# Kernel optimization log

Hardware: AMD Instinct MI355X
Metric: run time of the kernel (lower is better)

The kernel has to match this reference:

```python
import jax, jax.numpy as jnp
import numpy as np

B, R, VIS, MM, E, ATT, D, V, MAXLEN = 128, 36, 2048, 1024, 512, 512, 1024, 10000, 20


def setup_inputs() -> dict:
    key = jax.random.key(0)
    ks = jax.random.split(key, 16)
    s = 0.02
    visual = jax.random.normal(ks[0], (B, R, VIS), jnp.float32)
    joint = jax.random.normal(ks[1], (B, MM), jnp.float32)
    captions = jax.random.randint(ks[2], (B, MAXLEN), 0, V)
    # torch code requires lengths sorted descending (prefix slicing)
    lengths = jnp.sort(jax.random.randint(ks[3], (B,), 1, MAXLEN + 1))[::-1].astype(jnp.int32)
    embed_W = (jax.random.normal(ks[4], (V, E), jnp.float32) * s).at[0].set(0.0)  # padding_idx=0
    Wih = jax.random.normal(ks[5], (4 * D, E + VIS), jnp.float32) * s
    bih = jnp.zeros((4 * D,), jnp.float32)
    Whh = jax.random.normal(ks[6], (4 * D, D), jnp.float32) * s
    bhh = jnp.zeros((4 * D,), jnp.float32)
    W_init_h = jax.random.normal(ks[7], (D, MM), jnp.float32) * s
    b_init_h = jnp.zeros((D,), jnp.float32)
    W_init_c = jax.random.normal(ks[8], (D, MM), jnp.float32) * s
    b_init_c = jnp.zeros((D,), jnp.float32)
    Wv = jax.random.normal(ks[9], (ATT, VIS), jnp.float32) * s
    Wh = jax.random.normal(ks[10], (ATT, D), jnp.float32) * s
    att_bias = jnp.zeros((R,), jnp.float32)
    Ww = jax.random.normal(ks[11], (1, ATT), jnp.float32) * s
    Wout = jax.random.normal(ks[12], (V, D), jnp.float32) * s
    bout = jnp.zeros((V,), jnp.float32)
    return dict(visual=visual, joint=joint, captions=captions, lengths=lengths, max_len=MAXLEN,
                embed_W=embed_W, Wih=Wih, bih=bih, Whh=Whh, bhh=bhh,
                W_init_h=W_init_h, b_init_h=b_init_h, W_init_c=W_init_c, b_init_c=b_init_c,
                Wv=Wv, Wh=Wh, att_bias=att_bias, Ww=Ww, Wout=Wout, bout=bout)


def reference(visual, joint, captions, lengths, max_len, embed_W, Wih, bih, Whh, bhh,
              W_init_h, b_init_h, W_init_c, b_init_c, Wv, Wh, att_bias, Ww, Wout, bout):
    T = max_len - 1  # python int -> static scan length
    # dropout treated as identity (eval mode)
    words_seq = embed_W[captions[:, :T]]            # [B, T, E]
    h0 = joint @ W_init_h.T + b_init_h              # [B, D]
    c0 = joint @ W_init_c.T + b_init_c
    feas0 = visual.mean(axis=1)                     # [B, VIS]  (step 0 context)
    att_fea = jnp.einsum('brv,av->bra', visual, Wv)  # precompute visual projection
    lens = lengths.astype(jnp.int32)

    def step(carry, xs):
        h, c = carry
        t, words = xs
        # attention over 36 regions (used only when t != 0)
        ah = h @ Wh.T                                                   # [B, A]
        full = jax.nn.relu(att_fea + ah[:, None, :] + att_bias[None, :, None])
        alpha = jax.nn.softmax(jnp.einsum('bra,a->br', full, Ww[0]), axis=-1)
        ctx = jnp.einsum('br,brv->bv', alpha, visual)
        feas = jnp.where(t == 0, feas0, ctx)
        x = jnp.concatenate([feas, words], axis=-1)                     # [B, VIS+E]
        gates = x @ Wih.T + bih + h @ Whh.T + bhh                       # [B, 4D]
        i_, f_, g_, o_ = jnp.split(gates, 4, axis=-1)
        c_new = jax.nn.sigmoid(f_) * c + jax.nn.sigmoid(i_) * jnp.tanh(g_)
        h_new = jax.nn.sigmoid(o_) * jnp.tanh(c_new)
        mask = (t < lens)[:, None]                                      # ragged mask == torch prefix slice
        out = h_new @ Wout.T + bout                                     # [B, V]
        return (jnp.where(mask, h_new, h), jnp.where(mask, c_new, c)), jnp.where(mask, out, 0.0)

    _, preds = jax.lax.scan(step, (h0, c0), (jnp.arange(T), jnp.swapaxes(words_seq, 0, 1)))
    return jnp.transpose(preds, (1, 0, 2))  # [B, T, V]
```

## Files before the change

kernel.cpp:

```cpp
#include <hip/hip_runtime.h>
#include <math.h>

#define B 128
#define R 36
#define VIS 2048
#define MM 1024
#define E 512
#define ATT 512
#define D 1024
#define V 10000
#define MAXLEN 20
#define T 19
#define G4 4096

typedef unsigned short bf16_t;
typedef __attribute__((ext_vector_type(8))) short short8;
typedef __attribute__((ext_vector_type(4))) float f32x4;
typedef __attribute__((ext_vector_type(4))) unsigned short ushort4v;

__device__ __forceinline__ bf16_t f2bf(float f) {
    unsigned u = __float_as_uint(f);
    u += 0x7fff + ((u >> 16) & 1);
    return (bf16_t)(u >> 16);
}
__device__ __forceinline__ float bf2f(bf16_t b) {
    return __uint_as_float(((unsigned)b) << 16);
}
__device__ __forceinline__ float sigmoidf_(float x) { return 1.0f / (1.0f + expf(-x)); }

__device__ __forceinline__ void stage16(const bf16_t* g, bf16_t* lds_wave_base, int lane) {
#if defined(__has_builtin) && __has_builtin(__builtin_amdgcn_global_load_lds)
    __builtin_amdgcn_global_load_lds(
        (const __attribute__((address_space(1))) void*)g,
        (__attribute__((address_space(3))) void*)lds_wave_base, 16, 0, 0);
#else
    *(short8*)(lds_wave_base + lane * 8) = *(const short8*)g;
#endif
}

template<int MODE>
__global__ __launch_bounds__(256) void mfma_gemm_lds(
    const bf16_t* __restrict__ A, const bf16_t* __restrict__ W,
    const float* __restrict__ bias, const int* __restrict__ lengths,
    float* __restrict__ C, int M, int N, int K, int ldc,
    const float* __restrict__ bias2, float* __restrict__ C2,
    bf16_t* __restrict__ C3)
{
    __shared__ __align__(16) bf16_t As[128 * 32];
    __shared__ __align__(16) bf16_t Ws[128 * 32];
    const int tid = threadIdx.x;
    const int wave = tid >> 6, lane = tid & 63;
    const int wm = wave >> 1, wn = wave & 1;
    const int quad = lane >> 4, l16 = lane & 15;
    const int m0 = blockIdx.y * 128;
    const int n0 = blockIdx.x * 128;
    if (MODE == 2 && n0 >= N) return;

    int cnt = 128;
    if constexpr (MODE == 2) {
        const int tt = blockIdx.y;
        cnt = __syncthreads_count(tid < B && lengths[tid] > tt);
    }

    f32x4 acc[4][4];
    #pragma unroll
    for (int i = 0; i < 4; ++i)
        #pragma unroll
        for (int j = 0; j < 4; ++j)
            acc[i][j] = (f32x4){0.f, 0.f, 0.f, 0.f};

    for (int kk = 0; kk < K; kk += 32) {
        #pragma unroll
        for (int i = 0; i < 2; ++i) {
            int c = tid + i * 256;
            int row = c >> 2, seg = c & 3;
            if (MODE != 2 || (i * 64 + wave * 16) < cnt) {
                int m = m0 + row; if (m >= M) m = M - 1;
                stage16(A + (size_t)m * K + kk + seg * 8, &As[(i * 256 + wave * 64) * 8], lane);
            }
            int n = n0 + row; if (n >= N) n = N - 1;
            stage16(W + (size_t)n * K + kk + seg * 8, &Ws[(i * 256 + wave * 64) * 8], lane);
        }
        __syncthreads();
        short8 af[4], bfr[4];
        #pragma unroll
        for (int fm = 0; fm < 4; ++fm) {
            const int rt = (MODE == 2) ? fm * 2 + wm : wm * 4 + fm;
            if (MODE != 2 || rt * 16 < cnt)
                af[fm] = *(const short8*)&As[(rt * 16 + l16) * 32 + quad * 8];
        }
        #pragma unroll
        for (int fn = 0; fn < 4; ++fn)
            bfr[fn] = *(const short8*)&Ws[(wn * 64 + fn * 16 + l16) * 32 + quad * 8];
        #pragma unroll
        for (int fm = 0; fm < 4; ++fm) {
            const int rt = (MODE == 2) ? fm * 2 + wm : wm * 4 + fm;
            if (MODE == 2 && rt * 16 >= cnt) continue;
            #pragma unroll
            for (int fn = 0; fn < 4; ++fn)
                acc[fm][fn] = __builtin_amdgcn_mfma_f32_16x16x32_bf16(
                    af[fm], bfr[fn], acc[fm][fn], 0, 0, 0);
        }
        __syncthreads();
    }

    #pragma unroll
    for (int fm = 0; fm < 4; ++fm) {
        const int rt = (MODE == 2) ? fm * 2 + wm : wm * 4 + fm;
        #pragma unroll
        for (int fn = 0; fn < 4; ++fn) {
            #pragma unroll
            for (int r = 0; r < 4; ++r) {
                int m = m0 + rt * 16 + quad * 4 + r;
                int n = n0 + wn * 64 + fn * 16 + l16;
                if (m >= M || n >= N) continue;
                float v = acc[fm][fn][r];
                if (MODE == 0) {
                    if (bias) v += bias[n];
                    C[(size_t)m * ldc + n] = v;
                } else if (MODE == 2) {
                    int t = m >> 7, b = m & 127;
                    v = (t < lengths[b]) ? (v + bias[n]) : 0.f;
                    C[((size_t)b * T + t) * V + n] = v;
                } else if (MODE == 4) {
                    if (n < D) {
                        float v2 = v + bias[n];
                        C[(size_t)m * D + n] = v2;
                        C3[(size_t)m * D + n] = f2bf(v2);
                    } else {
                        C2[(size_t)m * D + (n - D)] = v + bias2[n - D];
                    }
                } else {
                    ((bf16_t*)C)[(size_t)m * ldc + n] = f2bf(v);
                }
            }
        }
    }
}

__global__ __launch_bounds__(256) void mfma_ah(
    const bf16_t* __restrict__ h_in,
    const bf16_t* __restrict__ Wh_pk,
    float* __restrict__ ah)
{
    __shared__ __align__(16) bf16_t Ws[32 * 1024];
    const int tid = threadIdx.x;
    const int wave = tid >> 6, lane = tid & 63;
    const int quad = lane >> 4, l16 = lane & 15;
    const int a0 = blockIdx.x * 32;
    const int m0 = blockIdx.y * 64;

    const bf16_t* slab = Wh_pk + ((size_t)blockIdx.x << 15);
    #pragma unroll
    for (int i = 0; i < 16; ++i) {
        int c = i * 256 + tid;
        stage16(slab + (size_t)c * 8, &Ws[(i * 256 + wave * 64) * 8], lane);
    }
    const bf16_t* Ar = h_in + (size_t)(m0 + wave * 16 + l16) * D + quad * 8;
    f32x4 acc0 = (f32x4){0.f, 0.f, 0.f, 0.f};
    f32x4 acc1 = (f32x4){0.f, 0.f, 0.f, 0.f};
    __syncthreads();

    #pragma unroll 8
    for (int kt = 0; kt < 32; ++kt) {
        short8 af = *(const short8*)(Ar + kt * 32);
        const int cb = (kt * 4 + quad) * 32 * 8;
        short8 b0 = *(const short8*)&Ws[cb + l16 * 8];
        short8 b1 = *(const short8*)&Ws[cb + (16 + l16) * 8];
        acc0 = __builtin_amdgcn_mfma_f32_16x16x32_bf16(af, b0, acc0, 0, 0, 0);
        acc1 = __builtin_amdgcn_mfma_f32_16x16x32_bf16(af, b1, acc1, 0, 0, 0);
    }
    #pragma unroll
    for (int r = 0; r < 4; ++r) {
        int m = m0 + wave * 16 + quad * 4 + r;
        ah[(size_t)m * ATT + a0 + l16]      = acc0[r];
        ah[(size_t)m * ATT + a0 + 16 + l16] = acc1[r];
    }
}

__global__ __launch_bounds__(256) void att_sc_p(
    const float* __restrict__ ah, const float* __restrict__ att_fea,
    const float* __restrict__ att_bias, const float* __restrict__ Ww,
    const bf16_t* __restrict__ P_bf, const float* __restrict__ wordsW,
    float* __restrict__ partial, int t)
{
    const int b = blockIdx.x, half = blockIdx.y, tid = threadIdx.x;
    __shared__ float ah_s[ATT];
    __shared__ float sc_s[64];
    __shared__ float alpha_s[R];
    const int wave = tid >> 6, lane = tid & 63;

    if (t > 0) {
        if (tid < 128) ((float4*)ah_s)[tid] = ((const float4*)(ah + (size_t)b * ATT))[tid];
        __syncthreads();
        for (int r = wave; r < R; r += 4) {
            float abv = att_bias[r];
            const float* af = att_fea + ((size_t)b * R + r) * ATT;
            float s = 0.f;
            for (int a = lane; a < ATT; a += 64) {
                float v = af[a] + ah_s[a] + abv;
                s = fmaf(fmaxf(v, 0.f), Ww[a], s);
            }
            #pragma unroll
            for (int off = 32; off; off >>= 1) s += __shfl_down(s, off);
            if (lane == 0) sc_s[r] = s;
        }
        __syncthreads();
        if (tid < 64) {
            float v = (tid < R) ? sc_s[tid] : -INFINITY;
            float m = v;
            #pragma unroll
            for (int off = 32; off; off >>= 1) m = fmaxf(m, __shfl_down(m, off));
            m = __shfl(m, 0);
            float e = (tid < R) ? expf(v - m) : 0.f;
            float ss = e;
            #pragma unroll
            for (int off = 32; off; off >>= 1) ss += __shfl_down(ss, off);
            ss = __shfl(ss, 0);
            if (tid < R) alpha_s[tid] = e / ss;
        }
        __syncthreads();
    }

    const int n0c = half * 2048 + tid * 8;
    float acc[8];
    #pragma unroll
    for (int j = 0; j < 8; ++j) acc[j] = 0.f;
    const bf16_t* Pb = P_bf + (size_t)b * R * G4 + n0c;
    #pragma unroll 4
    for (int r = 0; r < R; ++r) {
        float al = (t == 0) ? (1.0f / R) : alpha_s[r];
        short8 p = *(const short8*)(Pb + (size_t)r * G4);
        #pragma unroll
        for (int j = 0; j < 8; ++j)
            acc[j] = fmaf(al, bf2f((bf16_t)p[j]), acc[j]);
    }
    const float* wsl = wordsW + ((size_t)t * B + b) * G4 + n0c;
    float* po = partial + (size_t)b * G4 + n0c;
    float4 w0 = *(const float4*)(wsl);
    float4 w1 = *(const float4*)(wsl + 4);
    float4 o0 = { acc[0] + w0.x, acc[1] + w0.y, acc[2] + w0.z, acc[3] + w0.w };
    float4 o1 = { acc[4] + w1.x, acc[5] + w1.y, acc[6] + w1.z, acc[7] + w1.w };
    *(float4*)(po)     = o0;
    *(float4*)(po + 4) = o1;
}

__global__ __launch_bounds__(256) void whh_pack_k(
    const bf16_t* __restrict__ Whh, bf16_t* __restrict__ pk)
{
    int idx = blockIdx.x * 256 + threadIdx.x;
    int dt = idx >> 12, c = idx & 4095;
    int row = c & 31, qk = c >> 5;
    int rv = (row >> 3) * D + dt * 8 + (row & 7);
    *(short8*)(pk + ((size_t)dt << 15) + (size_t)c * 8) =
        *(const short8*)(Whh + (size_t)rv * D + qk * 8);
}

__global__ __launch_bounds__(256) void wh_pack_k(
    const bf16_t* __restrict__ Wh, bf16_t* __restrict__ pk)
{
    int idx = blockIdx.x * 256 + threadIdx.x;
    int at = idx >> 12, c = idx & 4095;
    int row = c & 31, qk = c >> 5;
    *(short8*)(pk + ((size_t)at << 15) + (size_t)c * 8) =
        *(const short8*)(Wh + (size_t)(at * 32 + row) * D + qk * 8);
}

__global__ __launch_bounds__(256) void gates_lstm(
    const bf16_t* __restrict__ h_in,
    const bf16_t* __restrict__ Whh_pk,
    const float* __restrict__ bih, const float* __restrict__ bhh,
    const float* __restrict__ partial,
    const int* __restrict__ lengths,
    float* __restrict__ c_st,
    float* __restrict__ h_f32,
    bf16_t* __restrict__ h_out,
    bf16_t* __restrict__ hseq,
    int t)
{
    __shared__ __align__(16) bf16_t Ws[32 * 1024];
    const int tid = threadIdx.x;
    const int wave = tid >> 6, lane = tid & 63;
    const int quad = lane >> 4, l16 = lane & 15;
    const int d0 = blockIdx.x * 8;
    const int m0 = blockIdx.y * 64;
    const int gsel_ = l16 >> 3, dr = l16 & 7;

    const bf16_t* slab = Whh_pk + ((size_t)blockIdx.x << 15);
    #pragma unroll
    for (int i = 0; i < 16; ++i) {
        int c = i * 256 + tid;
        stage16(slab + (size_t)c * 8, &Ws[(i * 256 + wave * 64) * 8], lane);
    }

    const bf16_t* Ar = h_in + (size_t)(m0 + wave * 16 + l16) * D + quad * 8;

    f32x4 acc0 = (f32x4){0.f, 0.f, 0.f, 0.f};
    f32x4 acc1 = (f32x4){0.f, 0.f, 0.f, 0.f};
    __syncthreads();

    #pragma unroll 8
    for (int kt = 0; kt < 32; ++kt) {
        short8 af = *(const short8*)(Ar + kt * 32);
        const int cb = (kt * 4 + quad) * 32 * 8;
        short8 b0 = *(const short8*)&Ws[cb + l16 * 8];
        short8 b1 = *(const short8*)&Ws[cb + (16 + l16) * 8];
        acc0 = __builtin_amdgcn_mfma_f32_16x16x32_bf16(af, b0, acc0, 0, 0, 0);
        acc1 = __builtin_amdgcn_mfma_f32_16x16x32_bf16(af, b1, acc1, 0, 0, 0);
    }

    const int d = d0 + dr;
    const int col0 = gsel_ * D + d;
    const int col1 = (2 + gsel_) * D + d;
    const float bia0 = bih[col0] + bhh[col0];
    const float bia1 = bih[col1] + bhh[col1];

    #pragma unroll
    for (int r = 0; r < 4; ++r) {
        int m = m0 + wave * 16 + quad * 4 + r;
        size_t pb = (size_t)m * G4;
        float v0 = acc0[r] + bia0 + partial[pb + col0];
        float v1 = acc1[r] + bia1 + partial[pb + col1];
        float w0 = __shfl_xor(v0, 8);
        float w1 = __shfl_xor(v1, 8);
        float iv, fv, gv, ov;
        if (gsel_ == 0) { iv = v0; gv = v1; fv = w0; ov = w1; }
        else            { fv = v0; ov = v1; iv = w0; gv = w1; }
        float ig = sigmoidf_(iv), fg = sigmoidf_(fv);
        float gg = tanhf(gv),     og = sigmoidf_(ov);
        size_t off = (size_t)m * D + d;
        if (gsel_ == 0) {
            float c_old = c_st[off];
            float h_old = h_f32[off];
            float cn = fmaf(fg, c_old, ig * gg);
            float hn = og * tanhf(cn);
            bool msk = t < lengths[m];
            float cv = msk ? cn : c_old;
            float hv = msk ? hn : h_old;
            c_st[off] = cv;
            h_f32[off] = hv;
            bf16_t hb = f2bf(hv);
            h_out[off] = hb;
            hseq[((size_t)t * B + m) * D + d] = hb;
        }
    }
}

struct CastSeg { const float* s; bf16_t* d; int cols; int ld; int total4; int blk0; };
struct Cast10 { CastSeg g[10]; };

__global__ __launch_bounds__(256) void fused_cast_k(Cast10 a)
{
    const int bx = blockIdx.x;
    CastSeg sg = a.g[0];
    #pragma unroll
    for (int j = 1; j < 10; ++j) if (bx >= a.g[j].blk0) sg = a.g[j];
    int idx = (bx - sg.blk0) * 256 + threadIdx.x;
    if (idx >= sg.total4) return;
    int cq = sg.cols >> 2;
    int r = idx / cq, c4 = (idx - r * cq) * 4;
    float4 v = *(const float4*)(sg.s + (size_t)r * sg.ld + c4);
    ushort4v o = { f2bf(v.x), f2bf(v.y), f2bf(v.z), f2bf(v.w) };
    *(ushort4v*)(sg.d + (size_t)r * sg.cols + c4) = o;
}

__global__ __launch_bounds__(128) void embed_k(
    const int* __restrict__ captions, const float* __restrict__ embed_W,
    bf16_t* __restrict__ words_bf)
{
    int bt = blockIdx.x;
    int b = bt / T, t = bt - b * T;
    int tok = captions[b * MAXLEN + t];
    int i = threadIdx.x * 4;
    float4 v = *(const float4*)(embed_W + (size_t)tok * E + i);
    ushort4v o = { f2bf(v.x), f2bf(v.y), f2bf(v.z), f2bf(v.w) };
    *(ushort4v*)(words_bf + ((size_t)t * B + b) * E + i) = o;
}

extern "C" void kernel_launch(void* const* d_in, const int* in_sizes, int n_in,
                              void* d_out, int out_size, void* d_ws, size_t ws_size,
                              hipStream_t stream) {
    const float* visual   = (const float*)d_in[0];
    const float* joint    = (const float*)d_in[1];
    const int*   captions = (const int*)d_in[2];
    const int*   lengths  = (const int*)d_in[3];
    const float* embed_W  = (const float*)d_in[5];
    const float* Wih      = (const float*)d_in[6];
    const float* bih      = (const float*)d_in[7];
    const float* Whh      = (const float*)d_in[8];
    const float* bhh      = (const float*)d_in[9];
    const float* W_init_h = (const float*)d_in[10];
    const float* b_init_h = (const float*)d_in[11];
    const float* W_init_c = (const float*)d_in[12];
    const float* b_init_c = (const float*)d_in[13];
    const float* Wv       = (const float*)d_in[14];
    const float* Wh       = (const float*)d_in[15];
    const float* att_bias = (const float*)d_in[16];
    const float* Ww       = (const float*)d_in[17];
    const float* Wout     = (const float*)d_in[18];
    const float* bout     = (const float*)d_in[19];
    float* out = (float*)d_out;

    char* cur = (char*)d_ws;
    auto alloc = [&](size_t bytes) { char* p = cur; cur += (bytes + 15) & ~size_t(15); return p; };
    float*  att_fea  = (float*)alloc((size_t)B * R * ATT * 4);
    float*  wordsW   = (float*)alloc((size_t)T * B * G4 * 4);
    float*  partial  = (float*)alloc((size_t)B * G4 * 4);
    float*  hf       = (float*)alloc((size_t)B * D * 4);
    float*  c_st     = (float*)alloc((size_t)B * D * 4);
    float*  ah       = (float*)alloc((size_t)B * ATT * 4);
    bf16_t* words_bf = (bf16_t*)alloc((size_t)T * B * E * 2);
    bf16_t* h_ping0  = (bf16_t*)alloc((size_t)B * D * 2);
    bf16_t* h_ping1  = (bf16_t*)alloc((size_t)B * D * 2);
    bf16_t* hseq_bf  = (bf16_t*)alloc((size_t)T * B * D * 2);
    bf16_t* P_bf     = (bf16_t*)alloc((size_t)B * R * G4 * 2);
    bf16_t* visual_bf= (bf16_t*)alloc((size_t)B * R * VIS * 2);
    bf16_t* Wv_bf    = (bf16_t*)alloc((size_t)ATT * VIS * 2);
    bf16_t* Wh_bf    = (bf16_t*)alloc((size_t)ATT * D * 2);
    bf16_t* Wh_pk    = (bf16_t*)alloc((size_t)ATT * D * 2);
    bf16_t* Whh_bf   = (bf16_t*)alloc((size_t)G4 * D * 2);
    bf16_t* Whh_pk   = (bf16_t*)alloc((size_t)G4 * D * 2);
    bf16_t* Wih_v_bf = (bf16_t*)alloc((size_t)G4 * VIS * 2);
    bf16_t* Wih_w_bf = (bf16_t*)alloc((size_t)G4 * E * 2);
    bf16_t* Wout_bf  = (bf16_t*)alloc((size_t)V * D * 2);
    bf16_t* joint_bf = (bf16_t*)alloc((size_t)B * MM * 2);
    bf16_t* Winit_bf = (bf16_t*)alloc((size_t)2 * D * MM * 2);

    Cast10 ca;
    int cum = 0;
    auto seg = [&](int i, const float* s, bf16_t* d, int rows, int cols, int ld) {
        int t4 = rows * (cols >> 2);
        ca.g[i] = { s, d, cols, ld, t4, cum };
        cum += (t4 + 255) / 256;
    };
    seg(0, visual, visual_bf, 1, B * R * VIS, B * R * VIS);
    seg(1, Wv,  Wv_bf,  ATT, VIS, VIS);
    seg(2, Wh,  Wh_bf,  ATT, D, D);
    seg(3, Whh, Whh_bf, G4, D, D);
    seg(4, Wih, Wih_v_bf, G4, VIS, VIS + E);
    seg(5, Wih + VIS, Wih_w_bf, G4, E, VIS + E);
    seg(6, Wout, Wout_bf, V, D, D);
    seg(7, joint, joint_bf, 1, B * MM, B * MM);
    seg(8, W_init_h, Winit_bf, 1, D * MM, D * MM);
    seg(9, W_init_c, Winit_bf + (size_t)D * MM, 1, D * MM, D * MM);
    fused_cast_k<<<cum, 256, 0, stream>>>(ca);

    whh_pack_k<<<(128 * 4096) / 256, 256, 0, stream>>>(Whh_bf, Whh_pk);
    wh_pack_k<<<(16 * 4096) / 256, 256, 0, stream>>>(Wh_bf, Wh_pk);
    embed_k<<<B * T, 128, 0, stream>>>(captions, embed_W, words_bf);

    mfma_gemm_lds<4><<<dim3(16, 1), 256, 0, stream>>>(
        joint_bf, Winit_bf, b_init_h, nullptr, hf, B, 2 * D, MM, D,
        b_init_c, c_st, h_ping0);

    mfma_gemm_lds<0><<<dim3(ATT / 128, (B * R) / 128), 256, 0, stream>>>(
        visual_bf, Wv_bf, nullptr, nullptr, att_fea, B * R, ATT, VIS, ATT,
        nullptr, nullptr, nullptr);

    mfma_gemm_lds<0><<<dim3(G4 / 128, (T * B) / 128), 256, 0, stream>>>(
        words_bf, Wih_w_bf, nullptr, nullptr, wordsW, T * B, G4, E, G4,
        nullptr, nullptr, nullptr);

    mfma_gemm_lds<3><<<dim3(G4 / 128, (B * R) / 128), 256, 0, stream>>>(
        visual_bf, Wih_v_bf, nullptr, nullptr, (float*)P_bf, B * R, G4, VIS, G4,
        nullptr, nullptr, nullptr);

    bf16_t* h_buf[2] = { h_ping0, h_ping1 };
    for (int t = 0; t < T; ++t) {
        if (t > 0)
            mfma_ah<<<dim3(ATT / 32, B / 64), 256, 0, stream>>>(
                h_buf[t & 1], Wh_pk, ah);
        att_sc_p<<<dim3(B, 2), 256, 0, stream>>>(
            ah, att_fea, att_bias, Ww, P_bf, wordsW, partial, t);
        gates_lstm<<<dim3(D / 8, B / 64), 256, 0, stream>>>(
            h_buf[t & 1], Whh_pk, bih, bhh, partial, lengths,
            c_st, hf, h_buf[(t + 1) & 1], hseq_bf, t);
    }

    mfma_gemm_lds<2><<<dim3(80, (T * B) / 128), 256, 0, stream>>>(
        hseq_bf, Wout_bf, bout, lengths, out, T * B, V, D, V,
        nullptr, nullptr, nullptr);
}
```

Measured before the change: 1.269 ms.

## Fuse attention scores into Wh GEMM and context into LSTM gates kernel

Each step's attention path is restructured. The scoring (relu, Ww dot) moves into the Wh MFMA kernel's epilogue, with per-tile partials combined by atomics into a per-step score buffer. The softmax, the alpha-weighted projected-context sum and the word term move into the gates kernel through a new d-tile-major packed layout of the visual×Wih product. This removes one kernel launch per step and the global round trips for ah and partial, at the cost of atomics, a memset and redundant softmax work per block. The MODE 2 staging skip for inactive rows is also dropped.

```diff
diff --git a/kernel.cpp b/kernel.cpp
--- a/kernel.cpp
+++ b/kernel.cpp
@@ -74,10 +74,8 @@
         for (int i = 0; i < 2; ++i) {
             int c = tid + i * 256;
             int row = c >> 2, seg = c & 3;
-            if (MODE != 2 || (i * 64 + wave * 16) < cnt) {
-                int m = m0 + row; if (m >= M) m = M - 1;
-                stage16(A + (size_t)m * K + kk + seg * 8, &As[(i * 256 + wave * 64) * 8], lane);
-            }
+            int m = m0 + row; if (m >= M) m = M - 1;
+            stage16(A + (size_t)m * K + kk + seg * 8, &As[(i * 256 + wave * 64) * 8], lane);
             int n = n0 + row; if (n >= N) n = N - 1;
             stage16(W + (size_t)n * K + kk + seg * 8, &Ws[(i * 256 + wave * 64) * 8], lane);
         }
@@ -130,6 +128,11 @@
                     } else {
                         C2[(size_t)m * D + (n - D)] = v + bias2[n - D];
                     }
+                } else if (MODE == 5) {
+                    int b = m / R, r2 = m - b * R;
+                    int dt = (n & 1023) >> 3;
+                    int c = ((n >> 10) << 3) | (n & 7);
+                    C3[((((size_t)dt * B + b) * R + r2) << 5) + c] = f2bf(v);
                 } else {
                     ((bf16_t*)C)[(size_t)m * ldc + n] = f2bf(v);
                 }
@@ -138,10 +141,10 @@
     }
 }
 
-__global__ __launch_bounds__(256) void mfma_ah(
-    const bf16_t* __restrict__ h_in,
-    const bf16_t* __restrict__ Wh_pk,
-    float* __restrict__ ah)
+__global__ __launch_bounds__(256) void ah_scores_k(
+    const bf16_t* __restrict__ h_in, const bf16_t* __restrict__ Wh_pk,
+    const float* __restrict__ att_fea, const float* __restrict__ att_bias,
+    const float* __restrict__ Ww, float* __restrict__ sc)
 {
     __shared__ __align__(16) bf16_t Ws[32 * 1024];
     const int tid = threadIdx.x;
@@ -170,131 +173,91 @@
         acc0 = __builtin_amdgcn_mfma_f32_16x16x32_bf16(af, b0, acc0, 0, 0, 0);
         acc1 = __builtin_amdgcn_mfma_f32_16x16x32_bf16(af, b1, acc1, 0, 0, 0);
     }
-    #pragma unroll
-    for (int r = 0; r < 4; ++r) {
-        int m = m0 + wave * 16 + quad * 4 + r;
-        ah[(size_t)m * ATT + a0 + l16]      = acc0[r];
-        ah[(size_t)m * ATT + a0 + 16 + l16] = acc1[r];
-    }
-}
-
-__global__ __launch_bounds__(256) void att_sc_p(
-    const float* __restrict__ ah, const float* __restrict__ att_fea,
-    const float* __restrict__ att_bias, const float* __restrict__ Ww,
-    const bf16_t* __restrict__ P_bf, const float* __restrict__ wordsW,
-    float* __restrict__ partial, int t)
-{
-    const int b = blockIdx.x, half = blockIdx.y, tid = threadIdx.x;
-    __shared__ float ah_s[ATT];
-    __shared__ float sc_s[64];
-    __shared__ float alpha_s[R];
-    const int wave = tid >> 6, lane = tid & 63;
-
-    if (t > 0) {
-        if (tid < 128) ((float4*)ah_s)[tid] = ((const float4*)(ah + (size_t)b * ATT))[tid];
-        __syncthreads();
-        for (int r = wave; r < R; r += 4) {
-            float abv = att_bias[r];
-            const float* af = att_fea + ((size_t)b * R + r) * ATT;
-            float s = 0.f;
-            for (int a = lane; a < ATT; a += 64) {
-                float v = af[a] + ah_s[a] + abv;
-                s = fmaf(fmaxf(v, 0.f), Ww[a], s);
-            }
-            #pragma unroll
-            for (int off = 32; off; off >>= 1) s += __shfl_down(s, off);
-            if (lane == 0) sc_s[r] = s;
-        }
-        __syncthreads();
-        if (tid < 64) {
-            float v = (tid < R) ? sc_s[tid] : -INFINITY;
-            float m = v;
-            #pragma unroll
-            for (int off = 32; off; off >>= 1) m = fmaxf(m, __shfl_down(m, off));
-            m = __shfl(m, 0);
-            float e = (tid < R) ? expf(v - m) : 0.f;
-            float ss = e;
-            #pragma unroll
-            for (int off = 32; off; off >>= 1) ss += __shfl_down(ss, off);
-            ss = __shfl(ss, 0);
-            if (tid < R) alpha_s[tid] = e / ss;
-        }
-        __syncthreads();
-    }
-
-    const int n0c = half * 2048 + tid * 8;
-    float acc[8];
-    #pragma unroll
-    for (int j = 0; j < 8; ++j) acc[j] = 0.f;
-    const bf16_t* Pb = P_bf + (size_t)b * R * G4 + n0c;
-    #pragma unroll 4
+    const float ww0 = Ww[a0 + l16], ww1 = Ww[a0 + 16 + l16];
+    const int mb = m0 + wave * 16 + quad * 4;
     for (int r = 0; r < R; ++r) {
-        float al = (t == 0) ? (1.0f / R) : alpha_s[r];
-        short8 p = *(const short8*)(Pb + (size_t)r * G4);
-        #pragma unroll
-        for (int j = 0; j < 8; ++j)
-            acc[j] = fmaf(al, bf2f((bf16_t)p[j]), acc[j]);
-    }
-    const float* wsl = wordsW + ((size_t)t * B + b) * G4 + n0c;
-    float* po = partial + (size_t)b * G4 + n0c;
-    float4 w0 = *(const float4*)(wsl);
-    float4 w1 = *(const float4*)(wsl + 4);
-    float4 o0 = { acc[0] + w0.x, acc[1] + w0.y, acc[2] + w0.z, acc[3] + w0.w };
-    float4 o1 = { acc[4] + w1.x, acc[5] + w1.y, acc[6] + w1.z, acc[7] + w1.w };
-    *(float4*)(po)     = o0;
-    *(float4*)(po + 4) = o1;
-}
-
-__global__ __launch_bounds__(256) void whh_pack_k(
-    const bf16_t* __restrict__ Whh, bf16_t* __restrict__ pk)
-{
-    int idx = blockIdx.x * 256 + threadIdx.x;
-    int dt = idx >> 12, c = idx & 4095;
-    int row = c & 31, qk = c >> 5;
-    int rv = (row >> 3) * D + dt * 8 + (row & 7);
-    *(short8*)(pk + ((size_t)dt << 15) + (size_t)c * 8) =
-        *(const short8*)(Whh + (size_t)rv * D + qk * 8);
-}
-
-__global__ __launch_bounds__(256) void wh_pack_k(
-    const bf16_t* __restrict__ Wh, bf16_t* __restrict__ pk)
-{
-    int idx = blockIdx.x * 256 + threadIdx.x;
-    int at = idx >> 12, c = idx & 4095;
-    int row = c & 31, qk = c >> 5;
-    *(short8*)(pk + ((size_t)at << 15) + (size_t)c * 8) =
-        *(const short8*)(Wh + (size_t)(at * 32 + row) * D + qk * 8);
-}
-
-__global__ __launch_bounds__(256) void gates_lstm(
-    const bf16_t* __restrict__ h_in,
-    const bf16_t* __restrict__ Whh_pk,
+        const float ab = att_bias[r];
+        #pragma unroll
+        for (int rh = 0; rh < 4; ++rh) {
+            const float* af = att_fea + ((size_t)(mb + rh) * R + r) * ATT + a0;
+            float s = fmaxf(af[l16] + acc0[rh] + ab, 0.f) * ww0
+                    + fmaxf(af[16 + l16] + acc1[rh] + ab, 0.f) * ww1;
+            s += __shfl_xor(s, 1); s += __shfl_xor(s, 2);
+            s += __shfl_xor(s, 4); s += __shfl_xor(s, 8);
+            if (l16 == 0) atomicAdd(&sc[(size_t)(mb + rh) * R + r], s);
+        }
+    }
+}
+
+__global__ __launch_bounds__(256) void att_gates_k(
+    const bf16_t* __restrict__ h_in, const bf16_t* __restrict__ Whh_pk,
+    const float* __restrict__ sc, const bf16_t* __restrict__ P_pk,
+    const float* __restrict__ wordsW_t,
     const float* __restrict__ bih, const float* __restrict__ bhh,
-    const float* __restrict__ partial,
     const int* __restrict__ lengths,
-    float* __restrict__ c_st,
-    float* __restrict__ h_f32,
-    bf16_t* __restrict__ h_out,
-    bf16_t* __restrict__ hseq,
-    int t)
+    float* __restrict__ c_st, float* __restrict__ h_f32,
+    bf16_t* __restrict__ h_out, bf16_t* __restrict__ hseq, int t)
 {
     __shared__ __align__(16) bf16_t Ws[32 * 1024];
+    __shared__ float part_s[64 * 36];
     const int tid = threadIdx.x;
     const int wave = tid >> 6, lane = tid & 63;
     const int quad = lane >> 4, l16 = lane & 15;
-    const int d0 = blockIdx.x * 8;
+    const int dt = blockIdx.x, d0 = dt * 8;
     const int m0 = blockIdx.y * 64;
     const int gsel_ = l16 >> 3, dr = l16 & 7;
 
-    const bf16_t* slab = Whh_pk + ((size_t)blockIdx.x << 15);
+    const bf16_t* slab = Whh_pk + ((size_t)dt << 15);
     #pragma unroll
     for (int i = 0; i < 16; ++i) {
         int c = i * 256 + tid;
         stage16(slab + (size_t)c * 8, &Ws[(i * 256 + wave * 64) * 8], lane);
     }
 
+    const int m_loc = tid >> 2, sub = tid & 3;
+    float av[9];
+    if (t > 0) {
+        const float* sr = sc + (size_t)(m0 + m_loc) * R + sub * 9;
+        float mx = -INFINITY;
+        #pragma unroll
+        for (int j = 0; j < 9; ++j) { av[j] = sr[j]; mx = fmaxf(mx, av[j]); }
+        mx = fmaxf(mx, __shfl_xor(mx, 1));
+        mx = fmaxf(mx, __shfl_xor(mx, 2));
+        float sm = 0.f;
+        #pragma unroll
+        for (int j = 0; j < 9; ++j) { av[j] = expf(av[j] - mx); sm += av[j]; }
+        sm += __shfl_xor(sm, 1); sm += __shfl_xor(sm, 2);
+        float inv = 1.f / sm;
+        #pragma unroll
+        for (int j = 0; j < 9; ++j) av[j] *= inv;
+    }
+
+    const int cg = sub;
+    float a8[8];
+    #pragma unroll
+    for (int j = 0; j < 8; ++j) a8[j] = 0.f;
+    const bf16_t* Pb = P_pk + ((((size_t)dt * B + (m0 + m_loc)) * R) << 5) + cg * 8;
+    const int lgbase = lane & ~3;
+    #pragma unroll
+    for (int r = 0; r < R; ++r) {
+        float al = (t == 0) ? (1.0f / R) : __shfl(av[r % 9], lgbase + r / 9);
+        short8 p = *(const short8*)(Pb + r * 32);
+        #pragma unroll
+        for (int j = 0; j < 8; ++j)
+            a8[j] = fmaf(al, bf2f((bf16_t)p[j]), a8[j]);
+    }
+    {
+        const float* wsl = wordsW_t + (size_t)(m0 + m_loc) * G4 + cg * 1024 + d0;
+        float4 w0 = *(const float4*)wsl;
+        float4 w1 = *(const float4*)(wsl + 4);
+        float* ps = &part_s[m_loc * 36 + cg * 8];
+        ps[0] = a8[0] + w0.x; ps[1] = a8[1] + w0.y;
+        ps[2] = a8[2] + w0.z; ps[3] = a8[3] + w0.w;
+        ps[4] = a8[4] + w1.x; ps[5] = a8[5] + w1.y;
+        ps[6] = a8[6] + w1.z; ps[7] = a8[7] + w1.w;
+    }
+
     const bf16_t* Ar = h_in + (size_t)(m0 + wave * 16 + l16) * D + quad * 8;
-
     f32x4 acc0 = (f32x4){0.f, 0.f, 0.f, 0.f};
     f32x4 acc1 = (f32x4){0.f, 0.f, 0.f, 0.f};
     __syncthreads();
@@ -317,10 +280,10 @@
 
     #pragma unroll
     for (int r = 0; r < 4; ++r) {
-        int m = m0 + wave * 16 + quad * 4 + r;
-        size_t pb = (size_t)m * G4;
-        float v0 = acc0[r] + bia0 + partial[pb + col0];
-        float v1 = acc1[r] + bia1 + partial[pb + col1];
+        int ml = wave * 16 + quad * 4 + r;
+        int m = m0 + ml;
+        float v0 = acc0[r] + bia0 + part_s[ml * 36 + gsel_ * 8 + dr];
+        float v1 = acc1[r] + bia1 + part_s[ml * 36 + 16 + gsel_ * 8 + dr];
         float w0 = __shfl_xor(v0, 8);
         float w1 = __shfl_xor(v1, 8);
         float iv, fv, gv, ov;
@@ -344,6 +307,27 @@
             hseq[((size_t)t * B + m) * D + d] = hb;
         }
     }
+}
+
+__global__ __launch_bounds__(256) void whh_pack_k(
+    const bf16_t* __restrict__ Whh, bf16_t* __restrict__ pk)
+{
+    int idx = blockIdx.x * 256 + threadIdx.x;
+    int dt = idx >> 12, c = idx & 4095;
+    int row = c & 31, qk = c >> 5;
+    int rv = (row >> 3) * D + dt * 8 + (row & 7);
+    *(short8*)(pk + ((size_t)dt << 15) + (size_t)c * 8) =
+        *(const short8*)(Whh + (size_t)rv * D + qk * 8);
+}
+
+__global__ __launch_bounds__(256) void wh_pack_k(
+    const bf16_t* __restrict__ Wh, bf16_t* __restrict__ pk)
+{
+    int idx = blockIdx.x * 256 + threadIdx.x;
+    int at = idx >> 12, c = idx & 4095;
+    int row = c & 31, qk = c >> 5;
+    *(short8*)(pk + ((size_t)at << 15) + (size_t)c * 8) =
+        *(const short8*)(Wh + (size_t)(at * 32 + row) * D + qk * 8);
 }
 
 struct CastSeg { const float* s; bf16_t* d; int cols; int ld; int total4; int blk0; };
@@ -405,15 +389,14 @@
     auto alloc = [&](size_t bytes) { char* p = cur; cur += (bytes + 15) & ~size_t(15); return p; };
     float*  att_fea  = (float*)alloc((size_t)B * R * ATT * 4);
     float*  wordsW   = (float*)alloc((size_t)T * B * G4 * 4);
-    float*  partial  = (float*)alloc((size_t)B * G4 * 4);
     float*  hf       = (float*)alloc((size_t)B * D * 4);
     float*  c_st     = (float*)alloc((size_t)B * D * 4);
-    float*  ah       = (float*)alloc((size_t)B * ATT * 4);
+    float*  sc_t     = (float*)alloc((size_t)T * B * R * 4);
     bf16_t* words_bf = (bf16_t*)alloc((size_t)T * B * E * 2);
     bf16_t* h_ping0  = (bf16_t*)alloc((size_t)B * D * 2);
     bf16_t* h_ping1  = (bf16_t*)alloc((size_t)B * D * 2);
     bf16_t* hseq_bf  = (bf16_t*)alloc((size_t)T * B * D * 2);
-    bf16_t* P_bf     = (bf16_t*)alloc((size_t)B * R * G4 * 2);
+    bf16_t* P_pk     = (bf16_t*)alloc((size_t)B * R * G4 * 2);
     bf16_t* visual_bf= (bf16_t*)alloc((size_t)B * R * VIS * 2);
     bf16_t* Wv_bf    = (bf16_t*)alloc((size_t)ATT * VIS * 2);
     bf16_t* Wh_bf    = (bf16_t*)alloc((size_t)ATT * D * 2);
@@ -448,6 +431,7 @@
     whh_pack_k<<<(128 * 4096) / 256, 256, 0, stream>>>(Whh_bf, Whh_pk);
     wh_pack_k<<<(16 * 4096) / 256, 256, 0, stream>>>(Wh_bf, Wh_pk);
     embed_k<<<B * T, 128, 0, stream>>>(captions, embed_W, words_bf);
+    hipMemsetAsync(sc_t, 0, (size_t)T * B * R * 4, stream);
 
     mfma_gemm_lds<4><<<dim3(16, 1), 256, 0, stream>>>(
         joint_bf, Winit_bf, b_init_h, nullptr, hf, B, 2 * D, MM, D,
@@ -461,20 +445,19 @@
         words_bf, Wih_w_bf, nullptr, nullptr, wordsW, T * B, G4, E, G4,
         nullptr, nullptr, nullptr);
 
-    mfma_gemm_lds<3><<<dim3(G4 / 128, (B * R) / 128), 256, 0, stream>>>(
-        visual_bf, Wih_v_bf, nullptr, nullptr, (float*)P_bf, B * R, G4, VIS, G4,
-        nullptr, nullptr, nullptr);
+    mfma_gemm_lds<5><<<dim3(G4 / 128, (B * R) / 128), 256, 0, stream>>>(
+        visual_bf, Wih_v_bf, nullptr, nullptr, nullptr, B * R, G4, VIS, G4,
+        nullptr, nullptr, P_pk);
 
     bf16_t* h_buf[2] = { h_ping0, h_ping1 };
     for (int t = 0; t < T; ++t) {
+        float* sct = sc_t + (size_t)t * B * R;
         if (t > 0)
-            mfma_ah<<<dim3(ATT / 32, B / 64), 256, 0, stream>>>(
-                h_buf[t & 1], Wh_pk, ah);
-        att_sc_p<<<dim3(B, 2), 256, 0, stream>>>(
-            ah, att_fea, att_bias, Ww, P_bf, wordsW, partial, t);
-        gates_lstm<<<dim3(D / 8, B / 64), 256, 0, stream>>>(
-            h_buf[t & 1], Whh_pk, bih, bhh, partial, lengths,
-            c_st, hf, h_buf[(t + 1) & 1], hseq_bf, t);
+            ah_scores_k<<<dim3(ATT / 32, B / 64), 256, 0, stream>>>(
+                h_buf[t & 1], Wh_pk, att_fea, att_bias, Ww, sct);
+        att_gates_k<<<dim3(D / 8, B / 64), 256, 0, stream>>>(
+            h_buf[t & 1], Whh_pk, sct, P_pk, wordsW + (size_t)t * B * G4,
+            bih, bhh, lengths, c_st, hf, h_buf[(t + 1) & 1], hseq_bf, t);
     }
 
     mfma_gemm_lds<2><<<dim3(80, (T * B) / 128), 256, 0, stream>>>(
```

Result: slower. 2.382 ms (+87.8%).
